# Kernel optimization log

Measured on AMD Instinct MI355X. Metric: run time of the kernel, lower is better.

## Reference

```python
import jax, jax.numpy as jnp
import numpy as np

SPATIAL_SCALE = 0.25
INV = int(1.0 / SPATIAL_SCALE)  # kernel_size == stride == 4


def _downsample_flow(flows, conv_w):
    # Fixed-weight strided conv: per-channel sum over INVxINV window * scale^3
    return jax.lax.conv_general_dilated(
        flows, conv_w, window_strides=(INV, INV), padding='VALID',
        dimension_numbers=('NCHW', 'OIHW', 'NCHW'))


def _warp_one(feat, flow):
    # feat: [C,H,W]; flow: [2,H,W] (x-displacement, y-displacement)
    C, H, W = feat.shape
    gx = jnp.arange(W, dtype=flow.dtype)[None, :] + flow[0]  # [H,W]
    gy = jnp.arange(H, dtype=flow.dtype)[:, None] + flow[1]  # [H,W]
    x0 = jnp.floor(gx)
    y0 = jnp.floor(gy)
    wx = gx - x0
    wy = gy - y0
    x0i = x0.astype(jnp.int32); x1i = x0i + 1
    y0i = y0.astype(jnp.int32); y1i = y0i + 1
    feat_flat = feat.reshape(C, H * W)

    def corner(xi, yi, w):
        valid = (xi >= 0) & (xi < W) & (yi >= 0) & (yi < H)
        idx = jnp.clip(yi, 0, H - 1) * W + jnp.clip(xi, 0, W - 1)  # [H,W]
        g = jnp.take(feat_flat, idx.reshape(-1), axis=1).reshape(C, H, W)
        return g * (w * valid.astype(w.dtype))[None, :, :]

    return (corner(x0i, y0i, (1 - wx) * (1 - wy))
            + corner(x1i, y0i, wx * (1 - wy))
            + corner(x0i, y1i, (1 - wx) * wy)
            + corner(x1i, y1i, wx * wy))


def setup_inputs() -> dict:
    key = jax.random.key(0)
    k1, k2 = jax.random.split(key)
    features = jax.random.normal(k1, (8, 256, 128, 128), dtype=jnp.float32)
    # flows at full resolution; scale so displacements span several pixels
    flows = jax.random.normal(k2, (8, 2, 512, 512), dtype=jnp.float32) * 8.0
    # fixed conv weights: diagonal entries = spatial_scale**3 (as in torch init)
    conv_w = jnp.zeros((2, 2, INV, INV), dtype=jnp.float32)
    conv_w = conv_w.at[0, 0].set(SPATIAL_SCALE ** 3).at[1, 1].set(SPATIAL_SCALE ** 3)
    return {'features': features, 'flows': flows, 'conv_w': conv_w}


def reference(features, flows, conv_w):
    f = _downsample_flow(flows, conv_w)  # [B,2,h,w] matching features
    return jax.vmap(_warp_one)(features, f)
```

## Files before the change

kernel.cpp:

```cpp
#include <hip/hip_runtime.h>

#define B   8
#define C   256
#define H   128
#define W   128
#define HW  (H * W)
#define FH  512
#define FW  512

#define TR     16
#define SLOTS  24
#define HALO   3
#define SW     132
#define CG     16
#define RGN    (H / TR)
#define CGN    (C / CG)

typedef float f32x4v __attribute__((ext_vector_type(4)));

struct __attribute__((packed, aligned(4))) pf2 { float x, y; };

__global__ __launch_bounds__(256) void downsample_kernel(
    const float* __restrict__ flows,
    const float* __restrict__ conv_w,
    float* __restrict__ f)
{
    int idx = blockIdx.x * blockDim.x + threadIdx.x;
    if (idx >= B * 2 * H * W) return;
    int x = idx & (W - 1);
    int y = (idx >> 7) & (H - 1);
    int o = (idx >> 14) & 1;
    int b = idx >> 15;

    const float* fb = flows + (size_t)b * 2 * FH * FW;
    const float* cw = conv_w + o * 2 * 16;

    float acc = 0.f;
#pragma unroll
    for (int i = 0; i < 2; ++i) {
        const float* fi = fb + (size_t)i * FH * FW;
#pragma unroll
        for (int kh = 0; kh < 4; ++kh) {
            const float4 v = *reinterpret_cast<const float4*>(
                fi + (size_t)(4 * y + kh) * FW + 4 * x);
            const float* w = cw + i * 16 + kh * 4;
            acc += v.x * w[0] + v.y * w[1] + v.z * w[2] + v.w * w[3];
        }
    }
    f[idx] = acc;
}

__global__ __launch_bounds__(256, 3) void warp_kernel(
    const float* __restrict__ feat,
    const float* __restrict__ f,
    float* __restrict__ out)
{
    __shared__ __align__(16) float rows[2][2][SLOTS * SW];

    const int hw_bid = blockIdx.x;
    const int lin = (hw_bid & 7) * 128 + (hw_bid >> 3);
    const int rg = lin & (RGN - 1);
    const int cg = (lin >> 3) & (CGN - 1);
    const int b  = lin >> 7;

    const int tid = threadIdx.x;
    const int ybase = rg * TR;
    const int row0  = ybase - HALO;
    const int pixbase = ybase * W;

    const float* featb = feat + ((size_t)b * C + (size_t)cg * CG) * HW;
    float*       outc  = out  + ((size_t)b * C + (size_t)cg * CG) * HW + pixbase;
    const float* fx_p  = f + (size_t)(b * 2 + 0) * HW;
    const float* fy_p  = f + (size_t)(b * 2 + 1) * HW;

    int goff0, goff1, goff2, soff0, soff1, soff2;
    {
        const int c0 = tid, c1 = 256 + tid, c2 = 512 + tid;
        const int r0c = min(max(row0 + (c0 >> 5), 0), H - 1);
        const int r1c = min(max(row0 + (c1 >> 5), 0), H - 1);
        const int r2c = min(max(row0 + (c2 >> 5), 0), H - 1);
        goff0 = r0c * W + (c0 & 31) * 4;
        goff1 = r1c * W + (c1 & 31) * 4;
        goff2 = r2c * W + (c2 & 31) * 4;
        soff0 = (c0 >> 5) * SW + (c0 & 31) * 4;
        soff1 = (c1 >> 5) * SW + (c1 & 31) * 4;
        soff2 = (c2 >> 5) * SW + (c2 & 31) * 4;
    }

    f32x4v nx0, nx1, nx2, mx0, mx1, mx2;

#define PREF2(cA, cB) do {                                                    \
        const float* _pA = featb + (size_t)(cA) * HW;                         \
        const float* _pB = featb + (size_t)(cB) * HW;                         \
        asm volatile("global_load_dwordx4 %0, %1, off"                        \
                     : "=v"(nx0) : "v"(_pA + goff0) : "memory");              \
        asm volatile("global_load_dwordx4 %0, %1, off"                        \
                     : "=v"(nx1) : "v"(_pA + goff1) : "memory");              \
        asm volatile("global_load_dwordx4 %0, %1, off"                        \
                     : "=v"(nx2) : "v"(_pA + goff2) : "memory");              \
        asm volatile("global_load_dwordx4 %0, %1, off"                        \
                     : "=v"(mx0) : "v"(_pB + goff0) : "memory");              \
        asm volatile("global_load_dwordx4 %0, %1, off"                        \
                     : "=v"(mx1) : "v"(_pB + goff1) : "memory");              \
        asm volatile("global_load_dwordx4 %0, %1, off"                        \
                     : "=v"(mx2) : "v"(_pB + goff2) : "memory");              \
    } while (0)

#define STASH2(s) do {                                                        \
        float* _dA = &rows[(s)][0][0];                                        \
        float* _dB = &rows[(s)][1][0];                                        \
        *reinterpret_cast<f32x4v*>(_dA + soff0) = nx0;                        \
        *reinterpret_cast<f32x4v*>(_dA + soff1) = nx1;                        \
        *reinterpret_cast<f32x4v*>(_dA + soff2) = nx2;                        \
        *reinterpret_cast<f32x4v*>(_dB + soff0) = mx0;                        \
        *reinterpret_cast<f32x4v*>(_dB + soff1) = mx1;                        \
        *reinterpret_cast<f32x4v*>(_dB + soff2) = mx2;                        \
    } while (0)

    PREF2(0, 1);

#define PXDECL(k) int i0_##k, i1_##k; float w0_##k, w1_##k, w2_##k, w3_##k;
    PXDECL(0) PXDECL(1) PXDECL(2) PXDECL(3)
    PXDECL(4) PXDECL(5) PXDECL(6) PXDECL(7)

#define WCOMP(k) do {                                                         \
        const int px  = tid + ((k) << 8);                                     \
        const int gpx = pixbase + px;                                         \
        const int x = gpx & (W - 1);                                          \
        const int y = gpx >> 7;                                               \
        const float gx = (float)x + fx_p[gpx];                                \
        const float gy = (float)y + fy_p[gpx];                                \
        const float x0f = floorf(gx);                                         \
        const float y0f = floorf(gy);                                         \
        const float wx = gx - x0f;                                            \
        const float wy = gy - y0f;                                            \
        const int x0 = (int)x0f, y0 = (int)y0f;                               \
        const int y1 = y0 + 1;                                                \
        const float u0 = 1.f - wx, u1 = wx;                                   \
        float A, Bv;                                                          \
        if (x0 >= 0 && x0 <= W - 2)      { A = u0;  Bv = u1;  }               \
        else if (x0 == W - 1)            { A = 0.f; Bv = u0;  }               \
        else if (x0 == -1)               { A = u1;  Bv = 0.f; }               \
        else                             { A = 0.f; Bv = 0.f; }               \
        const int bx = min(max(x0, 0), W - 2);                                \
        const float vy0 = (y0 >= 0 && y0 < H) ? 1.f : 0.f;                    \
        const float vy1 = (y1 >= 0 && y1 < H) ? 1.f : 0.f;                    \
        const int cy0 = min(max(y0, 0), H - 1);                               \
        const int cy1 = min(max(y1, 0), H - 1);                               \
        const int s0 = cy0 - row0;                                            \
        const int s1 = cy1 - row0;                                            \
        const bool ok = (s0 >= 0) && (s1 < SLOTS);                            \
        const int cs0 = min(max(s0, 0), SLOTS - 1);                           \
        const int cs1 = min(max(s1, 0), SLOTS - 1);                           \
        i0_##k = (cs0 * SW + bx) | (ok ? 0 : (int)0x80000000);                \
        i1_##k = cs1 * SW + bx;                                               \
        const float wy0 = (1.f - wy) * vy0;                                   \
        const float wy1 = wy * vy1;                                           \
        w0_##k = A * wy0;  w1_##k = Bv * wy0;                                 \
        w2_##k = A * wy1;  w3_##k = Bv * wy1;                                 \
    } while (0)

    WCOMP(0); WCOMP(1); WCOMP(2); WCOMP(3);
    WCOMP(4); WCOMP(5); WCOMP(6); WCOMP(7);

    const int anybad =
        ((i0_0 | i0_1 | i0_2 | i0_3 | i0_4 | i0_5 | i0_6 | i0_7) < 0);

    asm volatile("s_waitcnt vmcnt(0)" ::: "memory");
    __builtin_amdgcn_sched_barrier(0);
    STASH2(0);
    __syncthreads();

#define FPX2(k, rbA, rbB, ocA, ocB) do {                                      \
        const int px = tid + ((k) << 8);                                      \
        const pf2 a0 = *reinterpret_cast<const pf2*>(&rbA[i0_##k]);           \
        const pf2 a1 = *reinterpret_cast<const pf2*>(&rbA[i1_##k]);           \
        const pf2 b0 = *reinterpret_cast<const pf2*>(&rbB[i0_##k]);           \
        const pf2 b1 = *reinterpret_cast<const pf2*>(&rbB[i1_##k]);           \
        ocA[px] = a0.x * w0_##k + a0.y * w1_##k                               \
                + a1.x * w2_##k + a1.y * w3_##k;                              \
        ocB[px] = b0.x * w0_##k + b0.y * w1_##k                               \
                + b1.x * w2_##k + b1.y * w3_##k;                              \
    } while (0)

#define SPX2(k, ocA, ocB, chA) do {                                           \
        const int px = tid + ((k) << 8);                                      \
        const int gpx = pixbase + px;                                         \
        const int x = gpx & (W - 1);                                          \
        const int y = gpx >> 7;                                               \
        const int x0 = (int)floorf((float)x + fx_p[gpx]);                     \
        const int y0 = (int)floorf((float)y + fy_p[gpx]);                     \
        const int bx  = min(max(x0, 0), W - 2);                               \
        const int cy0 = min(max(y0, 0), H - 1);                               \
        const int cy1 = min(max(y0 + 1, 0), H - 1);                           \
        const float* fA = featb + (size_t)(chA) * HW;                         \
        const float* fB = fA + HW;                                            \
        ocA[px] = fA[cy0 * W + bx]     * w0_##k + fA[cy0 * W + bx + 1] * w1_##k\
                + fA[cy1 * W + bx]     * w2_##k + fA[cy1 * W + bx + 1] * w3_##k;\
        ocB[px] = fB[cy0 * W + bx]     * w0_##k + fB[cy0 * W + bx + 1] * w1_##k\
                + fB[cy1 * W + bx]     * w2_##k + fB[cy1 * W + bx + 1] * w3_##k;\
    } while (0)

    for (int p = 0; p < CG / 2; ++p) {
        const int chA = 2 * p;
        if (p < CG / 2 - 1) PREF2(chA + 2, chA + 3);

        const float* rbA = &rows[p & 1][0][0];
        const float* rbB = &rows[p & 1][1][0];
        float* ocA = outc + (size_t)chA * HW;
        float* ocB = ocA + HW;
        if (__builtin_expect(anybad, 0)) {
            SPX2(0, ocA, ocB, chA); SPX2(1, ocA, ocB, chA);
            SPX2(2, ocA, ocB, chA); SPX2(3, ocA, ocB, chA);
            SPX2(4, ocA, ocB, chA); SPX2(5, ocA, ocB, chA);
            SPX2(6, ocA, ocB, chA); SPX2(7, ocA, ocB, chA);
        } else {
            FPX2(0, rbA, rbB, ocA, ocB); FPX2(1, rbA, rbB, ocA, ocB);
            FPX2(2, rbA, rbB, ocA, ocB); FPX2(3, rbA, rbB, ocA, ocB);
            FPX2(4, rbA, rbB, ocA, ocB); FPX2(5, rbA, rbB, ocA, ocB);
            FPX2(6, rbA, rbB, ocA, ocB); FPX2(7, rbA, rbB, ocA, ocB);
        }

        if (p < CG / 2 - 1) {
            asm volatile("s_waitcnt vmcnt(16)" ::: "memory");
            __builtin_amdgcn_sched_barrier(0);
            STASH2((p + 1) & 1);
            __syncthreads();
        }
    }
#undef PREF2
#undef STASH2
#undef PXDECL
#undef WCOMP
#undef FPX2
#undef SPX2
}

extern "C" void kernel_launch(void* const* d_in, const int* in_sizes, int n_in,
                              void* d_out, int out_size, void* d_ws, size_t ws_size,
                              hipStream_t stream)
{
    const float* features = (const float*)d_in[0];
    const float* flows    = (const float*)d_in[1];
    const float* conv_w   = (const float*)d_in[2];
    float*       out      = (float*)d_out;
    float*       f        = (float*)d_ws;

    downsample_kernel<<<1024, 256, 0, stream>>>(flows, conv_w, f);
    warp_kernel<<<1024, 256, 0, stream>>>(features, f, out);
}
```

Before: 60.69 us.

## Stage feature rows via direct global-to-LDS loads with 512-thread blocks

Feature rows are now prefetched with global_load_lds straight into shared memory instead of going through registers and explicit LDS stores. The row padding (SW=132) is dropped to match that instruction's contiguous layout. Blocks grow to 512 threads, so each thread handles 4 pixels instead of 8, and the waitcnt thresholds are adjusted to match. The aim is to cut VGPR pressure and store instructions and raise occupancy, at the risk of LDS bank conflicts without padding and a wait count that may not match the new load count.

```diff
diff --git a/kernel.cpp b/kernel.cpp
--- a/kernel.cpp
+++ b/kernel.cpp
@@ -11,12 +11,11 @@
 #define TR     16
 #define SLOTS  24
 #define HALO   3
-#define SW     132
 #define CG     16
 #define RGN    (H / TR)
 #define CGN    (C / CG)
-
-typedef float f32x4v __attribute__((ext_vector_type(4)));
+#define NT     512
+#define PXT    (TR * W / NT)
 
 struct __attribute__((packed, aligned(4))) pf2 { float x, y; };
 
@@ -50,12 +49,17 @@
     f[idx] = acc;
 }
 
-__global__ __launch_bounds__(256, 3) void warp_kernel(
+#define GLOAD_LDS(gsrc, ldst)                                                 \
+    __builtin_amdgcn_global_load_lds(                                         \
+        (const __attribute__((address_space(1))) void*)(gsrc),                \
+        (__attribute__((address_space(3))) void*)(ldst), 16, 0, 0)
+
+__global__ __launch_bounds__(NT, 6) void warp_kernel(
     const float* __restrict__ feat,
     const float* __restrict__ f,
     float* __restrict__ out)
 {
-    __shared__ __align__(16) float rows[2][2][SLOTS * SW];
+    __shared__ __align__(16) float rows[2][2][SLOTS * W];
 
     const int hw_bid = blockIdx.x;
     const int lin = (hw_bid & 7) * 128 + (hw_bid >> 3);
@@ -63,7 +67,12 @@
     const int cg = (lin >> 3) & (CGN - 1);
     const int b  = lin >> 7;
 
-    const int tid = threadIdx.x;
+    const int tid  = threadIdx.x;
+    const int lane = tid & 63;
+    const int wv   = tid >> 6;
+    const int wq   = wv & 3;
+    const int half = wv >> 2;
+
     const int ybase = rg * TR;
     const int row0  = ybase - HALO;
     const int pixbase = ybase * W;
@@ -73,58 +82,32 @@
     const float* fx_p  = f + (size_t)(b * 2 + 0) * HW;
     const float* fy_p  = f + (size_t)(b * 2 + 1) * HW;
 
-    int goff0, goff1, goff2, soff0, soff1, soff2;
+    int goffs0, goffs1, goffs2;
     {
-        const int c0 = tid, c1 = 256 + tid, c2 = 512 + tid;
-        const int r0c = min(max(row0 + (c0 >> 5), 0), H - 1);
-        const int r1c = min(max(row0 + (c1 >> 5), 0), H - 1);
-        const int r2c = min(max(row0 + (c2 >> 5), 0), H - 1);
-        goff0 = r0c * W + (c0 & 31) * 4;
-        goff1 = r1c * W + (c1 & 31) * 4;
-        goff2 = r2c * W + (c2 & 31) * 4;
-        soff0 = (c0 >> 5) * SW + (c0 & 31) * 4;
-        soff1 = (c1 >> 5) * SW + (c1 & 31) * 4;
-        soff2 = (c2 >> 5) * SW + (c2 & 31) * 4;
+        const int wc0 = wq * 3 + 0, wc1 = wq * 3 + 1, wc2 = wq * 3 + 2;
+        const int r0c = min(max(row0 + 2 * wc0 + (lane >> 5), 0), H - 1);
+        const int r1c = min(max(row0 + 2 * wc1 + (lane >> 5), 0), H - 1);
+        const int r2c = min(max(row0 + 2 * wc2 + (lane >> 5), 0), H - 1);
+        goffs0 = r0c * W + (lane & 31) * 4;
+        goffs1 = r1c * W + (lane & 31) * 4;
+        goffs2 = r2c * W + (lane & 31) * 4;
     }
 
-    f32x4v nx0, nx1, nx2, mx0, mx1, mx2;
-
-#define PREF2(cA, cB) do {                                                    \
-        const float* _pA = featb + (size_t)(cA) * HW;                         \
-        const float* _pB = featb + (size_t)(cB) * HW;                         \
-        asm volatile("global_load_dwordx4 %0, %1, off"                        \
-                     : "=v"(nx0) : "v"(_pA + goff0) : "memory");              \
-        asm volatile("global_load_dwordx4 %0, %1, off"                        \
-                     : "=v"(nx1) : "v"(_pA + goff1) : "memory");              \
-        asm volatile("global_load_dwordx4 %0, %1, off"                        \
-                     : "=v"(nx2) : "v"(_pA + goff2) : "memory");              \
-        asm volatile("global_load_dwordx4 %0, %1, off"                        \
-                     : "=v"(mx0) : "v"(_pB + goff0) : "memory");              \
-        asm volatile("global_load_dwordx4 %0, %1, off"                        \
-                     : "=v"(mx1) : "v"(_pB + goff1) : "memory");              \
-        asm volatile("global_load_dwordx4 %0, %1, off"                        \
-                     : "=v"(mx2) : "v"(_pB + goff2) : "memory");              \
-    } while (0)
-
-#define STASH2(s) do {                                                        \
-        float* _dA = &rows[(s)][0][0];                                        \
-        float* _dB = &rows[(s)][1][0];                                        \
-        *reinterpret_cast<f32x4v*>(_dA + soff0) = nx0;                        \
-        *reinterpret_cast<f32x4v*>(_dA + soff1) = nx1;                        \
-        *reinterpret_cast<f32x4v*>(_dA + soff2) = nx2;                        \
-        *reinterpret_cast<f32x4v*>(_dB + soff0) = mx0;                        \
-        *reinterpret_cast<f32x4v*>(_dB + soff1) = mx1;                        \
-        *reinterpret_cast<f32x4v*>(_dB + soff2) = mx2;                        \
-    } while (0)
-
-    PREF2(0, 1);
+#define PREF2(s, chA) do {                                                    \
+        const float* _cb = featb + (size_t)((chA) + half) * HW;               \
+        float* _pl = &rows[(s)][half][0];                                     \
+        GLOAD_LDS(_cb + goffs0, _pl + (wq * 3 + 0) * 256);                    \
+        GLOAD_LDS(_cb + goffs1, _pl + (wq * 3 + 1) * 256);                    \
+        GLOAD_LDS(_cb + goffs2, _pl + (wq * 3 + 2) * 256);                    \
+    } while (0)
+
+    PREF2(0, 0);
 
 #define PXDECL(k) int i0_##k, i1_##k; float w0_##k, w1_##k, w2_##k, w3_##k;
     PXDECL(0) PXDECL(1) PXDECL(2) PXDECL(3)
-    PXDECL(4) PXDECL(5) PXDECL(6) PXDECL(7)
 
 #define WCOMP(k) do {                                                         \
-        const int px  = tid + ((k) << 8);                                     \
+        const int px  = tid + ((k) << 9);                                     \
         const int gpx = pixbase + px;                                         \
         const int x = gpx & (W - 1);                                          \
         const int y = gpx >> 7;                                               \
@@ -152,8 +135,8 @@
         const bool ok = (s0 >= 0) && (s1 < SLOTS);                            \
         const int cs0 = min(max(s0, 0), SLOTS - 1);                           \
         const int cs1 = min(max(s1, 0), SLOTS - 1);                           \
-        i0_##k = (cs0 * SW + bx) | (ok ? 0 : (int)0x80000000);                \
-        i1_##k = cs1 * SW + bx;                                               \
+        i0_##k = (cs0 * W + bx) | (ok ? 0 : (int)0x80000000);                 \
+        i1_##k = cs1 * W + bx;                                                \
         const float wy0 = (1.f - wy) * vy0;                                   \
         const float wy1 = wy * vy1;                                           \
         w0_##k = A * wy0;  w1_##k = Bv * wy0;                                 \
@@ -161,18 +144,15 @@
     } while (0)
 
     WCOMP(0); WCOMP(1); WCOMP(2); WCOMP(3);
-    WCOMP(4); WCOMP(5); WCOMP(6); WCOMP(7);
-
-    const int anybad =
-        ((i0_0 | i0_1 | i0_2 | i0_3 | i0_4 | i0_5 | i0_6 | i0_7) < 0);
+
+    const int anybad = ((i0_0 | i0_1 | i0_2 | i0_3) < 0);
 
     asm volatile("s_waitcnt vmcnt(0)" ::: "memory");
     __builtin_amdgcn_sched_barrier(0);
-    STASH2(0);
     __syncthreads();
 
 #define FPX2(k, rbA, rbB, ocA, ocB) do {                                      \
-        const int px = tid + ((k) << 8);                                      \
+        const int px = tid + ((k) << 9);                                      \
         const pf2 a0 = *reinterpret_cast<const pf2*>(&rbA[i0_##k]);           \
         const pf2 a1 = *reinterpret_cast<const pf2*>(&rbA[i1_##k]);           \
         const pf2 b0 = *reinterpret_cast<const pf2*>(&rbB[i0_##k]);           \
@@ -184,7 +164,7 @@
     } while (0)
 
 #define SPX2(k, ocA, ocB, chA) do {                                           \
-        const int px = tid + ((k) << 8);                                      \
+        const int px = tid + ((k) << 9);                                      \
         const int gpx = pixbase + px;                                         \
         const int x = gpx & (W - 1);                                          \
         const int y = gpx >> 7;                                               \
@@ -203,7 +183,7 @@
 
     for (int p = 0; p < CG / 2; ++p) {
         const int chA = 2 * p;
-        if (p < CG / 2 - 1) PREF2(chA + 2, chA + 3);
+        if (p < CG / 2 - 1) PREF2((p + 1) & 1, chA + 2);
 
         const float* rbA = &rows[p & 1][0][0];
         const float* rbB = &rows[p & 1][1][0];
@@ -212,24 +192,18 @@
         if (__builtin_expect(anybad, 0)) {
             SPX2(0, ocA, ocB, chA); SPX2(1, ocA, ocB, chA);
             SPX2(2, ocA, ocB, chA); SPX2(3, ocA, ocB, chA);
-            SPX2(4, ocA, ocB, chA); SPX2(5, ocA, ocB, chA);
-            SPX2(6, ocA, ocB, chA); SPX2(7, ocA, ocB, chA);
         } else {
             FPX2(0, rbA, rbB, ocA, ocB); FPX2(1, rbA, rbB, ocA, ocB);
             FPX2(2, rbA, rbB, ocA, ocB); FPX2(3, rbA, rbB, ocA, ocB);
-            FPX2(4, rbA, rbB, ocA, ocB); FPX2(5, rbA, rbB, ocA, ocB);
-            FPX2(6, rbA, rbB, ocA, ocB); FPX2(7, rbA, rbB, ocA, ocB);
         }
 
         if (p < CG / 2 - 1) {
-            asm volatile("s_waitcnt vmcnt(16)" ::: "memory");
+            asm volatile("s_waitcnt vmcnt(8)" ::: "memory");
             __builtin_amdgcn_sched_barrier(0);
-            STASH2((p + 1) & 1);
             __syncthreads();
         }
     }
 #undef PREF2
-#undef STASH2
 #undef PXDECL
 #undef WCOMP
 #undef FPX2
@@ -247,5 +221,5 @@
     float*       f        = (float*)d_ws;
 
     downsample_kernel<<<1024, 256, 0, stream>>>(flows, conv_w, f);
-    warp_kernel<<<1024, 256, 0, stream>>>(features, f, out);
+    warp_kernel<<<1024, NT, 0, stream>>>(features, f, out);
 }
```

Result: slower. 62.03 us (+2.2%).
